# Kernel tuning notes

Hardware: AMD Instinct MI355X
Metric: run time of the kernel (lower is better)

Reference implementation:

```python
import jax, jax.numpy as jnp
import numpy as np


def setup_inputs() -> dict:
    key = jax.random.key(0)
    k1, k2 = jax.random.split(key)
    data1 = jax.random.normal(k1, (2, 4, 4096, 3), dtype=jnp.float32)
    data2 = jax.random.normal(k2, (2, 4, 4096, 3), dtype=jnp.float32)
    return {"data1": data1, "data2": data2, "dim": 0}


def reference(data1, data2, dim):
    # dim == 0 -> swapaxes(0, 0) is identity (default path, dist_type=False)
    if dim > 0:
        data1 = jnp.swapaxes(data1, 0, dim)
        data2 = jnp.swapaxes(data2, 0, dim)
    # pairwise euclidean distances: [B, T, N, M]
    diff = data1[..., :, None, :] - data2[..., None, :, :]
    d2_matrix = jnp.sqrt(jnp.sum(diff * diff, axis=-1))
    # nearest-neighbor distance per point in set1: [B, T, N]
    nn_dist = jnp.min(d2_matrix, axis=-1)
    # func_type == mean: reduce over (-2, -1) -> [B]
    return jnp.mean(nn_dist, axis=(-2, -1))
```

## Files before the change

kernel.cpp:

```cpp
#include <hip/hip_runtime.h>
#include <math.h>

constexpr int kB   = 2;
constexpr int kT   = 4;
constexpr int kBT  = kB * kT;
constexpr int kN   = 4096;
constexpr int kR   = 4;
constexpr int kBLK = 256;
constexpr int kSP1 = kR * kBLK;
constexpr int kS1C = kN / kSP1;
constexpr int kSP2 = 128;
constexpr int kS2C = kN / kSP2;
constexpr int kNG  = kSP2 / 4;


__global__ __launch_bounds__(kBLK, 4) void hd_partial(
    const float* __restrict__ d1, const float* __restrict__ d2,
    float* __restrict__ ws, float* __restrict__ out)
{
    const int blk = blockIdx.x;
    const int c2  = blk % kS2C;
    const int t2  = blk / kS2C;
    const int c1  = t2 % kS1C;
    const int bt  = t2 / kS1C;

    const int tid = threadIdx.x;

    if (blk == 0 && tid < kB) out[tid] = 0.0f;

    const int p0 = c1 * kSP1 + tid;
    const float* __restrict__ base1 = d1 + (size_t)bt * kN * 3;
    float nx[kR], ny[kR], nz[kR], q1[kR], m[kR];
#pragma unroll
    for (int k = 0; k < kR; ++k) {
        const int p = p0 + k * kBLK;
        const float x = base1[p * 3 + 0];
        const float y = base1[p * 3 + 1];
        const float z = base1[p * 3 + 2];
        nx[k] = -2.0f * x; ny[k] = -2.0f * y; nz[k] = -2.0f * z;
        q1[k] = fmaf(x, x, fmaf(y, y, z * z));
        m[k]  = 3.402823466e38f;
    }

    const float4* __restrict__ g2 =
        (const float4*)(d2 + (size_t)bt * kN * 3 + (size_t)c2 * kSP2 * 3);

#pragma unroll 4
    for (int g = 0; g < kNG; ++g) {
        const float4 A  = g2[3 * g + 0];
        const float4 Bv = g2[3 * g + 1];
        const float4 Cv = g2[3 * g + 2];
        const float px[4] = {A.x, A.w, Bv.z, Cv.y};
        const float py[4] = {A.y, Bv.x, Bv.w, Cv.z};
        const float pz[4] = {A.z, Bv.y, Cv.x, Cv.w};
        float s[4][kR];
#pragma unroll
        for (int j = 0; j < 4; ++j) {
            const float q2 = fmaf(px[j], px[j], fmaf(py[j], py[j], pz[j] * pz[j]));
#pragma unroll
            for (int k = 0; k < kR; ++k) {
                float t = fmaf(px[j], nx[k], q2);
                t = fmaf(py[j], ny[k], t);
                s[j][k] = fmaf(pz[j], nz[k], t);
            }
        }
#pragma unroll
        for (int k = 0; k < kR; ++k) {
            m[k] = fminf(m[k], fminf(s[0][k], s[1][k]));
            m[k] = fminf(m[k], fminf(s[2][k], s[3][k]));
        }
    }

    float* __restrict__ wrow = ws + ((size_t)c2 * kBT + bt) * kN;
#pragma unroll
    for (int k = 0; k < kR; ++k)
        wrow[p0 + k * kBLK] = fmaxf(m[k] + q1[k], 0.0f);
}

__global__ __launch_bounds__(256) void hd_reduce(
    const float4* __restrict__ ws4, float* __restrict__ out)
{
    const int bt   = blockIdx.x >> 2;
    const int quad = blockIdx.x & 3;
    const int tid  = threadIdx.x;

    const int p4 = quad * 256 + tid;
    float4 m4 = make_float4(3.402823466e38f, 3.402823466e38f,
                            3.402823466e38f, 3.402823466e38f);
#pragma unroll 8
    for (int c2 = 0; c2 < kS2C; ++c2) {
        const float4 v = ws4[((size_t)c2 * kBT + bt) * (kN / 4) + p4];
        m4.x = fminf(m4.x, v.x);
        m4.y = fminf(m4.y, v.y);
        m4.z = fminf(m4.z, v.z);
        m4.w = fminf(m4.w, v.w);
    }
    float sum = sqrtf(m4.x) + sqrtf(m4.y) + sqrtf(m4.z) + sqrtf(m4.w);

#pragma unroll
    for (int off = 32; off >= 1; off >>= 1)
        sum += __shfl_down(sum, off, 64);

    __shared__ float ls[4];
    if ((tid & 63) == 0) ls[tid >> 6] = sum;
    __syncthreads();
    if (tid == 0) {
        const float tot = ls[0] + ls[1] + ls[2] + ls[3];
        atomicAdd(&out[bt >> 2], tot * (1.0f / (kT * kN)));
    }
}

extern "C" void kernel_launch(void* const* d_in, const int* in_sizes, int n_in,
                              void* d_out, int out_size, void* d_ws, size_t ws_size,
                              hipStream_t stream) {
    const float* d1 = (const float*)d_in[0];
    const float* d2 = (const float*)d_in[1];
    float* out = (float*)d_out;
    float* ws = (float*)d_ws;

    hd_partial<<<dim3(kBT * kS1C * kS2C), dim3(kBLK), 0, stream>>>(d1, d2, ws, out);
    hd_reduce<<<dim3(kBT * 4), dim3(256), 0, stream>>>((const float4*)ws, out);
}
```

Measured before the change: 77.57 us.

## Reduce nearest-neighbor minima in-block instead of through a global workspace

Each block now owns 32 set-1 points and splits the 4096 set-2 points across 32 thread groups, then combines the minima with wave shuffles and shared memory. It computes sqrt and a partial sum inside the block and writes one value per block. A single-block final kernel replaces the atomic reduction. This removes the large per-chunk minima workspace and its global round trip. In exchange the grid is smaller (1024 blocks), each block does more work, and there is extra shuffle and sync overhead.

```diff
diff --git a/kernel.cpp b/kernel.cpp
--- a/kernel.cpp
+++ b/kernel.cpp
@@ -1,49 +1,43 @@
 #include <hip/hip_runtime.h>
 #include <math.h>
 
-constexpr int kB   = 2;
-constexpr int kT   = 4;
-constexpr int kBT  = kB * kT;
-constexpr int kN   = 4096;
-constexpr int kR   = 4;
-constexpr int kBLK = 256;
-constexpr int kSP1 = kR * kBLK;
-constexpr int kS1C = kN / kSP1;
-constexpr int kSP2 = 128;
-constexpr int kS2C = kN / kSP2;
-constexpr int kNG  = kSP2 / 4;
+constexpr int kB    = 2;
+constexpr int kT    = 4;
+constexpr int kBT   = kB * kT;
+constexpr int kN    = 4096;
+constexpr int kBLK  = 256;
+constexpr int kR    = 4;
+constexpr int kP1   = 32;
+constexpr int kCHK  = kN / kP1;
+constexpr int kREP  = kBLK * kR / kP1;
+constexpr int kD2T  = kN / kREP;
+constexpr int kNG   = kD2T / 4;
 
+__global__ __launch_bounds__(kBLK, 4) void hd_main(
+    const float* __restrict__ d1, const float* __restrict__ d2,
+    float* __restrict__ ws)
+{
+    const int blk  = blockIdx.x;
+    const int bt   = blk >> 7;
+    const int cbase = (blk & 127) * kP1;
+    const int tid  = threadIdx.x;
+    const int pset = tid & 7;
+    const int rep  = tid >> 3;
 
-__global__ __launch_bounds__(kBLK, 4) void hd_partial(
-    const float* __restrict__ d1, const float* __restrict__ d2,
-    float* __restrict__ ws, float* __restrict__ out)
-{
-    const int blk = blockIdx.x;
-    const int c2  = blk % kS2C;
-    const int t2  = blk / kS2C;
-    const int c1  = t2 % kS1C;
-    const int bt  = t2 / kS1C;
-
-    const int tid = threadIdx.x;
-
-    if (blk == 0 && tid < kB) out[tid] = 0.0f;
-
-    const int p0 = c1 * kSP1 + tid;
     const float* __restrict__ base1 = d1 + (size_t)bt * kN * 3;
-    float nx[kR], ny[kR], nz[kR], q1[kR], m[kR];
+    float nx[kR], ny[kR], nz[kR], m[kR];
 #pragma unroll
     for (int k = 0; k < kR; ++k) {
-        const int p = p0 + k * kBLK;
+        const int p = cbase + pset * 4 + k;
         const float x = base1[p * 3 + 0];
         const float y = base1[p * 3 + 1];
         const float z = base1[p * 3 + 2];
         nx[k] = -2.0f * x; ny[k] = -2.0f * y; nz[k] = -2.0f * z;
-        q1[k] = fmaf(x, x, fmaf(y, y, z * z));
         m[k]  = 3.402823466e38f;
     }
 
     const float4* __restrict__ g2 =
-        (const float4*)(d2 + (size_t)bt * kN * 3 + (size_t)c2 * kSP2 * 3);
+        (const float4*)(d2 + (size_t)bt * kN * 3 + (size_t)rep * kD2T * 3);
 
 #pragma unroll 4
     for (int g = 0; g < kNG; ++g) {
@@ -71,42 +65,58 @@
         }
     }
 
-    float* __restrict__ wrow = ws + ((size_t)c2 * kBT + bt) * kN;
 #pragma unroll
-    for (int k = 0; k < kR; ++k)
-        wrow[p0 + k * kBLK] = fmaxf(m[k] + q1[k], 0.0f);
+    for (int off = 8; off <= 32; off <<= 1) {
+#pragma unroll
+        for (int k = 0; k < kR; ++k)
+            m[k] = fminf(m[k], __shfl_xor(m[k], off, 64));
+    }
+
+    __shared__ float ls[4][kP1];
+    const int lane = tid & 63;
+    const int wav  = tid >> 6;
+    if (lane < 8) {
+#pragma unroll
+        for (int k = 0; k < kR; ++k) ls[wav][lane * 4 + k] = m[k];
+    }
+    __syncthreads();
+
+    float sum = 0.0f;
+    if (tid < kP1) {
+        const float v = fminf(fminf(ls[0][tid], ls[1][tid]),
+                              fminf(ls[2][tid], ls[3][tid]));
+        const int p = cbase + tid;
+        const float x = base1[p * 3 + 0];
+        const float y = base1[p * 3 + 1];
+        const float z = base1[p * 3 + 2];
+        const float q1 = fmaf(x, x, fmaf(y, y, z * z));
+        sum = sqrtf(fmaxf(v + q1, 0.0f));
+#pragma unroll
+        for (int off = 16; off >= 1; off >>= 1)
+            sum += __shfl_down(sum, off, 64);
+        if (tid == 0) ws[blk] = sum;
+    }
 }
 
-__global__ __launch_bounds__(256) void hd_reduce(
-    const float4* __restrict__ ws4, float* __restrict__ out)
+__global__ __launch_bounds__(1024) void hd_final(
+    const float* __restrict__ ws, float* __restrict__ out)
 {
-    const int bt   = blockIdx.x >> 2;
-    const int quad = blockIdx.x & 3;
-    const int tid  = threadIdx.x;
-
-    const int p4 = quad * 256 + tid;
-    float4 m4 = make_float4(3.402823466e38f, 3.402823466e38f,
-                            3.402823466e38f, 3.402823466e38f);
-#pragma unroll 8
-    for (int c2 = 0; c2 < kS2C; ++c2) {
-        const float4 v = ws4[((size_t)c2 * kBT + bt) * (kN / 4) + p4];
-        m4.x = fminf(m4.x, v.x);
-        m4.y = fminf(m4.y, v.y);
-        m4.z = fminf(m4.z, v.z);
-        m4.w = fminf(m4.w, v.w);
-    }
-    float sum = sqrtf(m4.x) + sqrtf(m4.y) + sqrtf(m4.z) + sqrtf(m4.w);
-
+    const int tid = threadIdx.x;
+    float sum = ws[tid];
 #pragma unroll
     for (int off = 32; off >= 1; off >>= 1)
         sum += __shfl_down(sum, off, 64);
 
-    __shared__ float ls[4];
+    __shared__ float ls[16];
     if ((tid & 63) == 0) ls[tid >> 6] = sum;
     __syncthreads();
     if (tid == 0) {
-        const float tot = ls[0] + ls[1] + ls[2] + ls[3];
-        atomicAdd(&out[bt >> 2], tot * (1.0f / (kT * kN)));
+        float a = 0.0f, b = 0.0f;
+#pragma unroll
+        for (int w = 0; w < 8; ++w) { a += ls[w]; b += ls[w + 8]; }
+        const float scale = 1.0f / (kT * kN);
+        out[0] = a * scale;
+        out[1] = b * scale;
     }
 }
 
@@ -118,6 +128,6 @@
     float* out = (float*)d_out;
     float* ws = (float*)d_ws;
 
-    hd_partial<<<dim3(kBT * kS1C * kS2C), dim3(kBLK), 0, stream>>>(d1, d2, ws, out);
-    hd_reduce<<<dim3(kBT * 4), dim3(256), 0, stream>>>((const float4*)ws, out);
+    hd_main<<<dim3(kBT * kCHK), dim3(kBLK), 0, stream>>>(d1, d2, ws);
+    hd_final<<<dim3(1), dim3(1024), 0, stream>>>(ws, out);
 }
```

New measurement: 72.31 us (median of 2 runs). 6.8% less time.
